# Optimization experiments

Hardware: AMD Instinct MI355X
Metric: run time of the kernel (lower is better)

Reference implementation:

```python
import jax, jax.numpy as jnp
import numpy as np

B, N, D = 32, 128, 64
E = N * N
EPS = 1e-5


def _bn(x, gamma, beta):
    # torch BatchNorm1d on (B, C, D): normalize per-channel over (batch, last dim)
    mean = jnp.mean(x, axis=(0, 2), keepdims=True)
    var = jnp.var(x, axis=(0, 2), keepdims=True)
    return (x - mean) * jax.lax.rsqrt(var + EPS) * gamma[None, :, None] + beta[None, :, None]


def _gat_layer(x, edge, Wh, We, Wp, Wa, gv, bv, ge, be):
    b, n, d = x.shape
    res = x
    z_h = jnp.einsum('bnd,od->bno', x, Wh)   # fc_h (torch Linear: y = x W^T)
    z_e = jnp.einsum('bed,od->beo', edge, We)  # fc_e
    # incidence matmuls are pure gathers: edge e = i*n + j
    z_src = jnp.broadcast_to(z_h[:, None, :, :], (b, n, n, d)).reshape(b, n * n, d)  # start: edge (i,j) <- node j
    z_dst = jnp.broadcast_to(z_h[:, :, None, :], (b, n, n, d)).reshape(b, n * n, d)  # end:   edge (i,j) <- node i
    z = jnp.concatenate([z_src, z_dst, z_e], axis=-1)  # (b, E, 3d)
    z_e_new = jnp.einsum('bec,oc->beo', z, Wp)  # fc_proj
    attn = jnp.einsum('bec,c->be', z, Wa[0])    # attn_fc -> (b, E)
    attn = jnp.where(attn >= 0, attn, 0.01 * attn)  # LeakyReLU(0.01)
    attn = jax.nn.softmax(attn.reshape(b, n, n), axis=2).reshape(b, n * n)  # softmax over sources j
    # scatter via end^T: node i <- sum_j attn[i,j] * z_src[i*n+j]
    agg = (attn[:, :, None] * z_src).reshape(b, n, n, d).sum(axis=2)
    x_new = jax.nn.elu(res + _bn(agg, gv, bv))
    edge_new = jax.nn.elu(_bn(z_e_new, ge, be))
    return x_new, edge_new


def setup_inputs():
    key = jax.random.key(0)
    ks = jax.random.split(key, 10)
    scale = float(np.sqrt(2.0 / D))
    return {
        'x': jax.random.normal(ks[0], (B, N, D), jnp.float32),
        'edge': jax.random.normal(ks[1], (B, E, D), jnp.float32),
        'Wh1': jax.random.normal(ks[2], (D, D), jnp.float32) * scale,
        'We1': jax.random.normal(ks[3], (D, D), jnp.float32) * scale,
        'Wp1': jax.random.normal(ks[4], (D, 3 * D), jnp.float32) * scale,
        'Wa1': jax.random.normal(ks[5], (1, 3 * D), jnp.float32) * scale,
        'Wh2': jax.random.normal(ks[6], (D, D), jnp.float32) * scale,
        'We2': jax.random.normal(ks[7], (D, D), jnp.float32) * scale,
        'Wp2': jax.random.normal(ks[8], (D, 3 * D), jnp.float32) * scale,
        'Wa2': jax.random.normal(ks[9], (1, 3 * D), jnp.float32) * scale,
        'gv1': jnp.ones((N,), jnp.float32), 'bv1': jnp.zeros((N,), jnp.float32),
        'ge1': jnp.ones((E,), jnp.float32), 'be1': jnp.zeros((E,), jnp.float32),
        'gv2': jnp.ones((N,), jnp.float32), 'bv2': jnp.zeros((N,), jnp.float32),
        'ge2': jnp.ones((E,), jnp.float32), 'be2': jnp.zeros((E,), jnp.float32),
    }


def reference(x, edge, Wh1, We1, Wp1, Wa1, Wh2, We2, Wp2, Wa2,
              gv1, bv1, ge1, be1, gv2, bv2, ge2, be2):
    x, edge = _gat_layer(x, edge, Wh1, We1, Wp1, Wa1, gv1, bv1, ge1, be1)
    x, edge = _gat_layer(x, edge, Wh2, We2, Wp2, Wa2, gv2, bv2, ge2, be2)
    return x, edge
```

## Files before the change

### kernel.cpp

```cpp
#include <hip/hip_runtime.h>
#include <math.h>

#define BB 32
#define NN 128
#define DD 64
#define EE (NN*NN)
#define EPSI 1e-5f

typedef __attribute__((ext_vector_type(8))) short bf16x8;
typedef __attribute__((ext_vector_type(4))) short s16x4;
typedef __attribute__((ext_vector_type(4))) float f32x4;

#define LGKM0() do { asm volatile("s_waitcnt lgkmcnt(0)" ::: "memory"); \
                     __builtin_amdgcn_sched_barrier(0); } while (0)

__device__ __forceinline__ short f2bf(float f) {
    union { float f; unsigned u; } v; v.f = f;
    unsigned u = v.u;
    unsigned r = (u + 0x7FFFu + ((u >> 16) & 1u)) >> 16;
    return (short)r;
}
__device__ __forceinline__ float elu(float v) {
    return v > 0.f ? v : __expf(v) - 1.f;
}

__global__ void k_fold(const float* __restrict__ Wp, const float* __restrict__ We,
                       const float* __restrict__ Wa,
                       short* __restrict__ Mbf, short* __restrict__ wbf)
{
    int t = blockIdx.x * 256 + threadIdx.x;
    int d = t >> 6, k = t & 63;
    float acc = 0.f;
    for (int o = 0; o < DD; ++o)
        acc += Wp[d*192 + 128 + o] * We[o*DD + k];
    Mbf[d*DD + k] = f2bf(acc);
    if (d == 0) {
        float aw = 0.f;
        for (int o = 0; o < DD; ++o)
            aw += Wa[128 + o] * We[o*DD + k];
        wbf[k] = f2bf(aw);
    }
}

__global__ void k_node(const float* __restrict__ x, const float* __restrict__ Wh,
                       const float* __restrict__ Wp, const float* __restrict__ Wa,
                       float* __restrict__ zh, float* __restrict__ PsT,
                       float* __restrict__ PdT, float* __restrict__ sO,
                       float* __restrict__ tO)
{
    int row = blockIdx.x;
    int b = row >> 7, n = row & 127;
    int d = threadIdx.x;
    __shared__ float xr[DD];
    __shared__ float zr[DD];
    xr[d] = x[row*DD + d];
    __syncthreads();
    float acc = 0.f;
#pragma unroll
    for (int k = 0; k < DD; ++k) acc += xr[k] * Wh[d*DD + k];
    zr[d] = acc;
    zh[row*DD + d] = acc;
    __syncthreads();
    float a0 = 0.f, a1 = 0.f;
#pragma unroll
    for (int o = 0; o < DD; ++o) {
        float z = zr[o];
        a0 += Wp[d*192 + o]      * z;
        a1 += Wp[d*192 + 64 + o] * z;
    }
    const int fi = ((b >> 4)*4 + (d >> 4))*256 + (((b >> 2) & 3)*16 + (d & 15))*4 + (b & 3);
    PsT[n*2048 + fi] = a0;
    PdT[n*2048 + fi] = a1;
    float sv = zr[d] * Wa[d];
    float tv = zr[d] * Wa[64 + d];
#pragma unroll
    for (int off = 32; off; off >>= 1) {
        sv += __shfl_xor(sv, off);
        tv += __shfl_xor(tv, off);
    }
    if (d == 0) { sO[row] = sv; tO[row] = tv; }
}

template <int INM, int OUTM>
__global__ __launch_bounds__(256, 4) void k_edge(
    const void* __restrict__ einv,
    const short* __restrict__ Mbf,
    const short* __restrict__ wbf,
    const float* __restrict__ PsT,
    const float* __restrict__ PdT,
    const float* __restrict__ ge, const float* __restrict__ be,
    void* __restrict__ eoutv, float* __restrict__ uout)
{
    __shared__ short As[4][32][72];
    const int t  = threadIdx.x;
    const int l  = t & 63;
    const int wv = t >> 6;
    const int lr = l & 15;
    const int lg = l >> 4;
    const int e0 = blockIdx.x * 4;
    const int e  = e0 + wv;
    const int i0 = e >> 7, j0 = e & 127;

    bf16x8 afr[2][2];
    if constexpr (INM == 0) {
        const float* ein = (const float*)einv;
        const int tq = (t >> 4) & 3;
        const int d0 = (t & 15) * 4;
        float4 sv[8];
#pragma unroll
        for (int it = 0; it < 8; ++it) {
            const int b = it*4 + wv;
            sv[it] = *reinterpret_cast<const float4*>(
                         ein + ((size_t)b*EE + e0 + tq)*DD + d0);
        }
#pragma unroll
        for (int it = 0; it < 8; ++it) {
            const int b = it*4 + wv;
            s16x4 o;
            o[0] = f2bf(sv[it].x); o[1] = f2bf(sv[it].y);
            o[2] = f2bf(sv[it].z); o[3] = f2bf(sv[it].w);
            *reinterpret_cast<s16x4*>(&As[tq][b][d0]) = o;
        }
        __syncthreads();
#pragma unroll
        for (int m = 0; m < 2; ++m)
#pragma unroll
            for (int s = 0; s < 2; ++s)
                afr[m][s] = *reinterpret_cast<const bf16x8*>(
                                &As[wv][16*m + lr][s*32 + lg*8]);
    } else {
        const short* ein = (const short*)einv + (size_t)e*BB*DD;
#pragma unroll
        for (int m = 0; m < 2; ++m)
#pragma unroll
            for (int s = 0; s < 2; ++s)
                afr[m][s] = *reinterpret_cast<const bf16x8*>(
                                ein + (16*m + lr)*DD + s*32 + lg*8);
    }

    bf16x8 bfr[4][2];
#pragma unroll
    for (int n = 0; n < 4; ++n)
#pragma unroll
        for (int s = 0; s < 2; ++s)
            bfr[n][s] = *reinterpret_cast<const bf16x8*>(Mbf + (16*n + lr)*DD + s*32 + lg*8);
    const bf16x8 zerov = (bf16x8){0,0,0,0,0,0,0,0};
    bf16x8 wfrag[2];
#pragma unroll
    for (int s = 0; s < 2; ++s)
        wfrag[s] = (lr == 0) ? *reinterpret_cast<const bf16x8*>(wbf + s*32 + lg*8) : zerov;

    f32x4 acc[2][4];
    f32x4 uacc[2];
    {
        const float* psb = PsT + j0*2048;
        const float* pdb = PdT + i0*2048;
#pragma unroll
        for (int m = 0; m < 2; ++m) {
            uacc[m] = (f32x4){0.f, 0.f, 0.f, 0.f};
#pragma unroll
            for (int n = 0; n < 4; ++n) {
                const float4 a = *reinterpret_cast<const float4*>(psb + (m*4+n)*256 + l*4);
                const float4 c = *reinterpret_cast<const float4*>(pdb + (m*4+n)*256 + l*4);
                acc[m][n] = (f32x4){a.x+c.x, a.y+c.y, a.z+c.z, a.w+c.w};
            }
        }
    }

#pragma unroll
    for (int m = 0; m < 2; ++m) {
#pragma unroll
        for (int n = 0; n < 4; ++n)
            acc[m][n] = __builtin_amdgcn_mfma_f32_16x16x32_bf16(afr[m][0], bfr[n][0], acc[m][n], 0, 0, 0);
        uacc[m] = __builtin_amdgcn_mfma_f32_16x16x32_bf16(afr[m][0], wfrag[0], uacc[m], 0, 0, 0);
#pragma unroll
        for (int n = 0; n < 4; ++n)
            acc[m][n] = __builtin_amdgcn_mfma_f32_16x16x32_bf16(afr[m][1], bfr[n][1], acc[m][n], 0, 0, 0);
        uacc[m] = __builtin_amdgcn_mfma_f32_16x16x32_bf16(afr[m][1], wfrag[1], uacc[m], 0, 0, 0);
    }

    float s1 = 0.f, s2 = 0.f;
#pragma unroll
    for (int m = 0; m < 2; ++m)
#pragma unroll
        for (int n = 0; n < 4; ++n)
#pragma unroll
            for (int q = 0; q < 4; ++q) { float v = acc[m][n][q]; s1 += v; s2 += v*v; }
#pragma unroll
    for (int off = 1; off < 64; off <<= 1) {
        s1 += __shfl_xor(s1, off);
        s2 += __shfl_xor(s2, off);
    }
    const float mean = s1 * (1.f/2048.f);
    const float var  = s2 * (1.f/2048.f) - mean*mean;
    const float sc = ge[e] * rsqrtf(var + EPSI);
    const float sh = be[e] - mean*sc;

#pragma unroll
    for (int m = 0; m < 2; ++m)
#pragma unroll
        for (int n = 0; n < 4; ++n)
#pragma unroll
            for (int q = 0; q < 4; ++q)
                acc[m][n][q] = elu(acc[m][n][q]*sc + sh);

    if (lr == 0) {
#pragma unroll
        for (int m = 0; m < 2; ++m)
#pragma unroll
            for (int q = 0; q < 4; ++q)
                uout[(size_t)(16*m + 4*lg + q)*EE + e] = uacc[m][q];
    }

    float (*Z)[68] = reinterpret_cast<float (*)[68]>(&As[wv][0][0]);
    LGKM0();
#pragma unroll
    for (int h = 0; h < 2; ++h) {
#pragma unroll
        for (int n = 0; n < 4; ++n)
#pragma unroll
            for (int q = 0; q < 4; ++q)
                Z[4*lg + q][16*n + lr] = acc[h][n][q];
        LGKM0();
        if constexpr (OUTM == 0) {
            float* eout = (float*)eoutv;
#pragma unroll
            for (int it = 0; it < 4; ++it) {
                const int rr = lg + 4*it;
                const int b  = 16*h + rr;
                float4 z = *reinterpret_cast<float4*>(&Z[rr][lr*4]);
                *reinterpret_cast<float4*>(eout + ((size_t)b*EE + e)*DD + lr*4) = z;
            }
        } else {
            short* eout = (short*)eoutv + (size_t)e*BB*DD;
#pragma unroll
            for (int it = 0; it < 2; ++it) {
                const int rr = (l >> 3) + 8*it;
                const int b  = 16*h + rr;
                const int c0 = (l & 7)*8;
                float4 zlo = *reinterpret_cast<float4*>(&Z[rr][c0]);
                float4 zhi = *reinterpret_cast<float4*>(&Z[rr][c0+4]);
                bf16x8 o;
                o[0]=f2bf(zlo.x); o[1]=f2bf(zlo.y); o[2]=f2bf(zlo.z); o[3]=f2bf(zlo.w);
                o[4]=f2bf(zhi.x); o[5]=f2bf(zhi.y); o[6]=f2bf(zhi.z); o[7]=f2bf(zhi.w);
                *reinterpret_cast<bf16x8*>(eout + b*DD + c0) = o;
            }
        }
        LGKM0();
    }
}

__global__ void k_attn(const float* __restrict__ sI, const float* __restrict__ tI,
                       const float* __restrict__ u, const float* __restrict__ zh,
                       float* __restrict__ agg)
{
    int blk = blockIdx.x; int b = blk >> 7, i = blk & 127;
    int l = threadIdx.x;
    __shared__ float at[NN];
    float ti = tI[blk];
    float l0 = sI[b*NN + l]      + ti + u[b*EE + i*NN + l];
    float l1 = sI[b*NN + l + 64] + ti + u[b*EE + i*NN + l + 64];
    l0 = l0 >= 0.f ? l0 : 0.01f*l0;
    l1 = l1 >= 0.f ? l1 : 0.01f*l1;
    float mx = fmaxf(l0, l1);
#pragma unroll
    for (int off = 32; off; off >>= 1) mx = fmaxf(mx, __shfl_xor(mx, off));
    float e0 = __expf(l0 - mx), e1 = __expf(l1 - mx);
    float sm = e0 + e1;
#pragma unroll
    for (int off = 32; off; off >>= 1) sm += __shfl_xor(sm, off);
    float inv = 1.f / sm;
    at[l]      = e0 * inv;
    at[l + 64] = e1 * inv;
    __syncthreads();
    float acc = 0.f;
    for (int j = 0; j < NN; ++j) acc += at[j] * zh[(b*NN + j)*DD + l];
    agg[(b*NN + i)*DD + l] = acc;
}

__global__ void k_vbn(const float* __restrict__ agg, const float* __restrict__ xres,
                      const float* __restrict__ gv, const float* __restrict__ bv,
                      float* __restrict__ xout)
{
    int i = blockIdx.x, t = threadIdx.x;
    float vals[8];
    float s1 = 0.f, s2 = 0.f;
#pragma unroll
    for (int q = 0; q < 8; ++q) {
        int m = t + 256*q; int b = m >> 6, d = m & 63;
        float v = agg[(b*NN + i)*DD + d];
        vals[q] = v; s1 += v; s2 += v*v;
    }
#pragma unroll
    for (int off = 1; off < 64; off <<= 1) {
        s1 += __shfl_xor(s1, off);
        s2 += __shfl_xor(s2, off);
    }
    __shared__ float r1[4], r2[4];
    int wv = t >> 6;
    if ((t & 63) == 0) { r1[wv] = s1; r2[wv] = s2; }
    __syncthreads();
    s1 = r1[0] + r1[1] + r1[2] + r1[3];
    s2 = r2[0] + r2[1] + r2[2] + r2[3];
    float mean  = s1 * (1.f/2048.f);
    float var   = s2 * (1.f/2048.f) - mean*mean;
    float scale = gv[i] * rsqrtf(var + EPSI);
    float shift = bv[i] - mean*scale;
#pragma unroll
    for (int q = 0; q < 8; ++q) {
        int m = t + 256*q; int b = m >> 6, d = m & 63;
        float v = vals[q]*scale + shift + xres[(b*NN + i)*DD + d];
        xout[(b*NN + i)*DD + d] = v > 0.f ? v : __expf(v) - 1.f;
    }
}

extern "C" void kernel_launch(void* const* d_in, const int* in_sizes, int n_in,
                              void* d_out, int out_size, void* d_ws, size_t ws_size,
                              hipStream_t stream)
{
    const float* x    = (const float*)d_in[0];
    const float* edge = (const float*)d_in[1];
    const float* Wh1  = (const float*)d_in[2];
    const float* We1  = (const float*)d_in[3];
    const float* Wp1  = (const float*)d_in[4];
    const float* Wa1  = (const float*)d_in[5];
    const float* Wh2  = (const float*)d_in[6];
    const float* We2  = (const float*)d_in[7];
    const float* Wp2  = (const float*)d_in[8];
    const float* Wa2  = (const float*)d_in[9];
    const float* gv1  = (const float*)d_in[10];
    const float* bv1  = (const float*)d_in[11];
    const float* ge1  = (const float*)d_in[12];
    const float* be1  = (const float*)d_in[13];
    const float* gv2  = (const float*)d_in[14];
    const float* bv2  = (const float*)d_in[15];
    const float* ge2  = (const float*)d_in[16];
    const float* be2  = (const float*)d_in[17];

    float* xout = (float*)d_out;
    float* eout = (float*)d_out + BB*NN*DD;

    float* ws  = (float*)d_ws;
    short* Mbf = (short*)ws;  ws += DD*DD/2;
    short* wbf = (short*)ws;  ws += DD/2;
    float* zh  = ws;  ws += BB*NN*DD;
    float* PsT = ws;  ws += NN*BB*DD;
    float* PdT = ws;  ws += NN*BB*DD;
    float* sb  = ws;  ws += BB*NN;
    float* tb  = ws;  ws += BB*NN;
    float* ub  = ws;  ws += BB*EE;
    float* agg = ws;  ws += BB*NN*DD;
    float* x1  = ws;  ws += BB*NN*DD;
    short* e1bf = (short*)ws;
    const size_t need = ((size_t)(ws - (float*)d_ws))*4 + (size_t)EE*BB*DD*2;

    const bool dense = (ws_size >= need);

    k_fold<<<16, 256, 0, stream>>>(Wp1, We1, Wa1, Mbf, wbf);
    k_node<<<BB*NN, 64, 0, stream>>>(x, Wh1, Wp1, Wa1, zh, PsT, PdT, sb, tb);
    if (dense)
        k_edge<0,1><<<EE/4, 256, 0, stream>>>(edge, Mbf, wbf, PsT, PdT, ge1, be1, e1bf, ub);
    else
        k_edge<0,0><<<EE/4, 256, 0, stream>>>(edge, Mbf, wbf, PsT, PdT, ge1, be1, eout, ub);
    k_attn<<<BB*NN, 64, 0, stream>>>(sb, tb, ub, zh, agg);
    k_vbn<<<NN, 256, 0, stream>>>(agg, x, gv1, bv1, x1);
    k_fold<<<16, 256, 0, stream>>>(Wp2, We2, Wa2, Mbf, wbf);
    k_node<<<BB*NN, 64, 0, stream>>>(x1, Wh2, Wp2, Wa2, zh, PsT, PdT, sb, tb);
    if (dense)
        k_edge<1,0><<<EE/4, 256, 0, stream>>>(e1bf, Mbf, wbf, PsT, PdT, ge2, be2, eout, ub);
    else
        k_edge<0,0><<<EE/4, 256, 0, stream>>>(eout, Mbf, wbf, PsT, PdT, ge2, be2, eout, ub);
    k_attn<<<BB*NN, 64, 0, stream>>>(sb, tb, ub, zh, agg);
    k_vbn<<<NN, 256, 0, stream>>>(agg, x1, gv2, bv2, xout);
}
```

Measured before the change: 208.6 us.

## Process two edges per wave, fold weight prep into node kernel, compute attention term in FP32

Each k_edge block now handles 8 edges (two per wave) instead of 4, which halves the grid and shares the PdT row and the Mbf fragments across both edges. The attention edge term u is now an FP32 dot product on the loaded edge data instead of an extra MFMA with a padded weight fragment. The separate k_fold launch is merged into k_node as extra blocks, removing two kernel launches. Register pressure goes up (launch bounds lowered from 4 to 3 blocks), shared memory per block doubles, and the shuffle reductions add ALU work.

```diff
diff --git a/kernel.cpp b/kernel.cpp
--- a/kernel.cpp
+++ b/kernel.cpp
@@ -20,37 +20,42 @@
     unsigned r = (u + 0x7FFFu + ((u >> 16) & 1u)) >> 16;
     return (short)r;
 }
+__device__ __forceinline__ float bf2f(short s) {
+    union { unsigned u; float f; } v; v.u = ((unsigned)(unsigned short)s) << 16;
+    return v.f;
+}
+__device__ __forceinline__ float dot4(float4 a, float4 b) {
+    return a.x*b.x + a.y*b.y + a.z*b.z + a.w*b.w;
+}
 __device__ __forceinline__ float elu(float v) {
     return v > 0.f ? v : __expf(v) - 1.f;
 }
 
-__global__ void k_fold(const float* __restrict__ Wp, const float* __restrict__ We,
+__global__ void k_node(const float* __restrict__ x, const float* __restrict__ Wh,
+                       const float* __restrict__ Wp, const float* __restrict__ We,
                        const float* __restrict__ Wa,
-                       short* __restrict__ Mbf, short* __restrict__ wbf)
-{
-    int t = blockIdx.x * 256 + threadIdx.x;
-    int d = t >> 6, k = t & 63;
-    float acc = 0.f;
-    for (int o = 0; o < DD; ++o)
-        acc += Wp[d*192 + 128 + o] * We[o*DD + k];
-    Mbf[d*DD + k] = f2bf(acc);
-    if (d == 0) {
-        float aw = 0.f;
-        for (int o = 0; o < DD; ++o)
-            aw += Wa[128 + o] * We[o*DD + k];
-        wbf[k] = f2bf(aw);
-    }
-}
-
-__global__ void k_node(const float* __restrict__ x, const float* __restrict__ Wh,
-                       const float* __restrict__ Wp, const float* __restrict__ Wa,
                        float* __restrict__ zh, float* __restrict__ PsT,
                        float* __restrict__ PdT, float* __restrict__ sO,
-                       float* __restrict__ tO)
+                       float* __restrict__ tO,
+                       short* __restrict__ Mbf, float* __restrict__ wf32)
 {
-    int row = blockIdx.x;
-    int b = row >> 7, n = row & 127;
-    int d = threadIdx.x;
+    const int row = blockIdx.x;
+    const int d = threadIdx.x;
+    if (row >= BB*NN) {
+        const int ff = row - BB*NN;
+        float acc = 0.f;
+        for (int o = 0; o < DD; ++o)
+            acc += Wp[ff*192 + 128 + o] * We[o*DD + d];
+        Mbf[ff*DD + d] = f2bf(acc);
+        if (ff == 0) {
+            float aw = 0.f;
+            for (int o = 0; o < DD; ++o)
+                aw += Wa[128 + o] * We[o*DD + d];
+            wf32[d] = aw;
+        }
+        return;
+    }
+    const int b = row >> 7, n = row & 127;
     __shared__ float xr[DD];
     __shared__ float zr[DD];
     xr[d] = x[row*DD + d];
@@ -82,60 +87,53 @@
 }
 
 template <int INM, int OUTM>
-__global__ __launch_bounds__(256, 4) void k_edge(
+__global__ __launch_bounds__(256, 3) void k_edge(
     const void* __restrict__ einv,
     const short* __restrict__ Mbf,
-    const short* __restrict__ wbf,
+    const float* __restrict__ wf32,
     const float* __restrict__ PsT,
     const float* __restrict__ PdT,
     const float* __restrict__ ge, const float* __restrict__ be,
     void* __restrict__ eoutv, float* __restrict__ uout)
 {
-    __shared__ short As[4][32][72];
+    __shared__ short As[8][32][72];
     const int t  = threadIdx.x;
     const int l  = t & 63;
     const int wv = t >> 6;
     const int lr = l & 15;
     const int lg = l >> 4;
-    const int e0 = blockIdx.x * 4;
-    const int e  = e0 + wv;
-    const int i0 = e >> 7, j0 = e & 127;
-
-    bf16x8 afr[2][2];
+    const int e0 = blockIdx.x * 8;
+    const int i0 = e0 >> 7;
+
     if constexpr (INM == 0) {
         const float* ein = (const float*)einv;
-        const int tq = (t >> 4) & 3;
+        const int g  = t >> 4;
         const int d0 = (t & 15) * 4;
-        float4 sv[8];
-#pragma unroll
-        for (int it = 0; it < 8; ++it) {
-            const int b = it*4 + wv;
+        const int el = g & 7;
+        const int bb = g >> 3;
+        const float4 wv4 = *reinterpret_cast<const float4*>(wf32 + d0);
+        float4 sv[16];
+#pragma unroll
+        for (int it = 0; it < 16; ++it) {
+            const int b = bb + 2*it;
             sv[it] = *reinterpret_cast<const float4*>(
-                         ein + ((size_t)b*EE + e0 + tq)*DD + d0);
-        }
-#pragma unroll
-        for (int it = 0; it < 8; ++it) {
-            const int b = it*4 + wv;
+                         ein + ((size_t)b*EE + e0 + el)*DD + d0);
+        }
+#pragma unroll
+        for (int it = 0; it < 16; ++it) {
+            const int b = bb + 2*it;
             s16x4 o;
             o[0] = f2bf(sv[it].x); o[1] = f2bf(sv[it].y);
             o[2] = f2bf(sv[it].z); o[3] = f2bf(sv[it].w);
-            *reinterpret_cast<s16x4*>(&As[tq][b][d0]) = o;
+            *reinterpret_cast<s16x4*>(&As[el][b][d0]) = o;
+            float up = dot4(sv[it], wv4);
+            up += __shfl_xor(up, 1);
+            up += __shfl_xor(up, 2);
+            up += __shfl_xor(up, 4);
+            up += __shfl_xor(up, 8);
+            if ((t & 15) == 0) uout[(size_t)b*EE + e0 + el] = up;
         }
         __syncthreads();
-#pragma unroll
-        for (int m = 0; m < 2; ++m)
-#pragma unroll
-            for (int s = 0; s < 2; ++s)
-                afr[m][s] = *reinterpret_cast<const bf16x8*>(
-                                &As[wv][16*m + lr][s*32 + lg*8]);
-    } else {
-        const short* ein = (const short*)einv + (size_t)e*BB*DD;
-#pragma unroll
-        for (int m = 0; m < 2; ++m)
-#pragma unroll
-            for (int s = 0; s < 2; ++s)
-                afr[m][s] = *reinterpret_cast<const bf16x8*>(
-                                ein + (16*m + lr)*DD + s*32 + lg*8);
     }
 
     bf16x8 bfr[4][2];
@@ -144,109 +142,157 @@
 #pragma unroll
         for (int s = 0; s < 2; ++s)
             bfr[n][s] = *reinterpret_cast<const bf16x8*>(Mbf + (16*n + lr)*DD + s*32 + lg*8);
-    const bf16x8 zerov = (bf16x8){0,0,0,0,0,0,0,0};
-    bf16x8 wfrag[2];
-#pragma unroll
-    for (int s = 0; s < 2; ++s)
-        wfrag[s] = (lr == 0) ? *reinterpret_cast<const bf16x8*>(wbf + s*32 + lg*8) : zerov;
-
-    f32x4 acc[2][4];
-    f32x4 uacc[2];
-    {
+
+    float4 wlo[2], whi[2];
+    if constexpr (INM == 1) {
+#pragma unroll
+        for (int s = 0; s < 2; ++s) {
+            wlo[s] = *reinterpret_cast<const float4*>(wf32 + s*32 + lg*8);
+            whi[s] = *reinterpret_cast<const float4*>(wf32 + s*32 + lg*8 + 4);
+        }
+    }
+
+    f32x4 acc[2][2][4];
+#pragma unroll
+    for (int ch = 0; ch < 2; ++ch) {
+        const int e  = e0 + 2*wv + ch;
+        const int j0 = e & 127;
         const float* psb = PsT + j0*2048;
         const float* pdb = PdT + i0*2048;
 #pragma unroll
-        for (int m = 0; m < 2; ++m) {
-            uacc[m] = (f32x4){0.f, 0.f, 0.f, 0.f};
+        for (int m = 0; m < 2; ++m)
 #pragma unroll
             for (int n = 0; n < 4; ++n) {
                 const float4 a = *reinterpret_cast<const float4*>(psb + (m*4+n)*256 + l*4);
                 const float4 c = *reinterpret_cast<const float4*>(pdb + (m*4+n)*256 + l*4);
-                acc[m][n] = (f32x4){a.x+c.x, a.y+c.y, a.z+c.z, a.w+c.w};
+                acc[ch][m][n] = (f32x4){a.x+c.x, a.y+c.y, a.z+c.z, a.w+c.w};
             }
-        }
-    }
-
-#pragma unroll
-    for (int m = 0; m < 2; ++m) {
+    }
+
+#pragma unroll
+    for (int ch = 0; ch < 2; ++ch) {
+        const int e = e0 + 2*wv + ch;
+        bf16x8 afr[2][2];
+        if constexpr (INM == 0) {
+#pragma unroll
+            for (int m = 0; m < 2; ++m)
+#pragma unroll
+                for (int s = 0; s < 2; ++s)
+                    afr[m][s] = *reinterpret_cast<const bf16x8*>(
+                                    &As[2*wv + ch][16*m + lr][s*32 + lg*8]);
+        } else {
+            const short* ein = (const short*)einv + (size_t)e*BB*DD;
+#pragma unroll
+            for (int m = 0; m < 2; ++m)
+#pragma unroll
+                for (int s = 0; s < 2; ++s)
+                    afr[m][s] = *reinterpret_cast<const bf16x8*>(
+                                    ein + (16*m + lr)*DD + s*32 + lg*8);
+#pragma unroll
+            for (int m = 0; m < 2; ++m) {
+                float up = 0.f;
+#pragma unroll
+                for (int s = 0; s < 2; ++s) {
+                    up += bf2f(afr[m][s][0])*wlo[s].x + bf2f(afr[m][s][1])*wlo[s].y
+                        + bf2f(afr[m][s][2])*wlo[s].z + bf2f(afr[m][s][3])*wlo[s].w
+                        + bf2f(afr[m][s][4])*whi[s].x + bf2f(afr[m][s][5])*whi[s].y
+                        + bf2f(afr[m][s][6])*whi[s].z + bf2f(afr[m][s][7])*whi[s].w;
+                }
+                up += __shfl_xor(up, 16);
+                up += __shfl_xor(up, 32);
+                if (lg == 0) uout[(size_t)(16*m + lr)*EE + e] = up;
+            }
+        }
+#pragma unroll
+        for (int m = 0; m < 2; ++m) {
+#pragma unroll
+            for (int n = 0; n < 4; ++n)
+                acc[ch][m][n] = __builtin_amdgcn_mfma_f32_16x16x32_bf16(afr[m][0], bfr[n][0], acc[ch][m][n], 0, 0, 0);
+#pragma unroll
+            for (int n = 0; n < 4; ++n)
+                acc[ch][m][n] = __builtin_amdgcn_mfma_f32_16x16x32_bf16(afr[m][1], bfr[n][1], acc[ch][m][n], 0, 0, 0);
+        }
+    }
+
+    float s1a = 0.f, s2a = 0.f, s1b = 0.f, s2b = 0.f;
+#pragma unroll
+    for (int m = 0; m < 2; ++m)
 #pragma unroll
         for (int n = 0; n < 4; ++n)
-            acc[m][n] = __builtin_amdgcn_mfma_f32_16x16x32_bf16(afr[m][0], bfr[n][0], acc[m][n], 0, 0, 0);
-        uacc[m] = __builtin_amdgcn_mfma_f32_16x16x32_bf16(afr[m][0], wfrag[0], uacc[m], 0, 0, 0);
-#pragma unroll
-        for (int n = 0; n < 4; ++n)
-            acc[m][n] = __builtin_amdgcn_mfma_f32_16x16x32_bf16(afr[m][1], bfr[n][1], acc[m][n], 0, 0, 0);
-        uacc[m] = __builtin_amdgcn_mfma_f32_16x16x32_bf16(afr[m][1], wfrag[1], uacc[m], 0, 0, 0);
-    }
-
-    float s1 = 0.f, s2 = 0.f;
-#pragma unroll
-    for (int m = 0; m < 2; ++m)
-#pragma unroll
-        for (int n = 0; n < 4; ++n)
-#pragma unroll
-            for (int q = 0; q < 4; ++q) { float v = acc[m][n][q]; s1 += v; s2 += v*v; }
+#pragma unroll
+            for (int q = 0; q < 4; ++q) {
+                float va = acc[0][m][n][q]; s1a += va; s2a += va*va;
+                float vb = acc[1][m][n][q]; s1b += vb; s2b += vb*vb;
+            }
 #pragma unroll
     for (int off = 1; off < 64; off <<= 1) {
-        s1 += __shfl_xor(s1, off);
-        s2 += __shfl_xor(s2, off);
-    }
-    const float mean = s1 * (1.f/2048.f);
-    const float var  = s2 * (1.f/2048.f) - mean*mean;
-    const float sc = ge[e] * rsqrtf(var + EPSI);
-    const float sh = be[e] - mean*sc;
-
-#pragma unroll
-    for (int m = 0; m < 2; ++m)
-#pragma unroll
-        for (int n = 0; n < 4; ++n)
-#pragma unroll
-            for (int q = 0; q < 4; ++q)
-                acc[m][n][q] = elu(acc[m][n][q]*sc + sh);
-
-    if (lr == 0) {
+        s1a += __shfl_xor(s1a, off);
+        s2a += __shfl_xor(s2a, off);
+        s1b += __shfl_xor(s1b, off);
+        s2b += __shfl_xor(s2b, off);
+    }
+    float scs[2], shs[2];
+    {
+        const int eA = e0 + 2*wv;
+        float mean = s1a * (1.f/2048.f);
+        float var  = s2a * (1.f/2048.f) - mean*mean;
+        scs[0] = ge[eA] * rsqrtf(var + EPSI);
+        shs[0] = be[eA] - mean*scs[0];
+        mean = s1b * (1.f/2048.f);
+        var  = s2b * (1.f/2048.f) - mean*mean;
+        scs[1] = ge[eA+1] * rsqrtf(var + EPSI);
+        shs[1] = be[eA+1] - mean*scs[1];
+    }
+
+#pragma unroll
+    for (int ch = 0; ch < 2; ++ch)
 #pragma unroll
         for (int m = 0; m < 2; ++m)
 #pragma unroll
-            for (int q = 0; q < 4; ++q)
-                uout[(size_t)(16*m + 4*lg + q)*EE + e] = uacc[m][q];
-    }
-
-    float (*Z)[68] = reinterpret_cast<float (*)[68]>(&As[wv][0][0]);
+            for (int n = 0; n < 4; ++n)
+#pragma unroll
+                for (int q = 0; q < 4; ++q)
+                    acc[ch][m][n][q] = elu(acc[ch][m][n][q]*scs[ch] + shs[ch]);
+
     LGKM0();
 #pragma unroll
-    for (int h = 0; h < 2; ++h) {
-#pragma unroll
-        for (int n = 0; n < 4; ++n)
-#pragma unroll
-            for (int q = 0; q < 4; ++q)
-                Z[4*lg + q][16*n + lr] = acc[h][n][q];
-        LGKM0();
-        if constexpr (OUTM == 0) {
-            float* eout = (float*)eoutv;
-#pragma unroll
-            for (int it = 0; it < 4; ++it) {
-                const int rr = lg + 4*it;
-                const int b  = 16*h + rr;
-                float4 z = *reinterpret_cast<float4*>(&Z[rr][lr*4]);
-                *reinterpret_cast<float4*>(eout + ((size_t)b*EE + e)*DD + lr*4) = z;
+    for (int ch = 0; ch < 2; ++ch) {
+        const int e = e0 + 2*wv + ch;
+        float (*Z)[68] = reinterpret_cast<float (*)[68]>(&As[2*wv + ch][0][0]);
+#pragma unroll
+        for (int h = 0; h < 2; ++h) {
+#pragma unroll
+            for (int n = 0; n < 4; ++n)
+#pragma unroll
+                for (int q = 0; q < 4; ++q)
+                    Z[4*lg + q][16*n + lr] = acc[ch][h][n][q];
+            LGKM0();
+            if constexpr (OUTM == 0) {
+                float* eout = (float*)eoutv;
+#pragma unroll
+                for (int it = 0; it < 4; ++it) {
+                    const int rr = lg + 4*it;
+                    const int b  = 16*h + rr;
+                    float4 z = *reinterpret_cast<float4*>(&Z[rr][lr*4]);
+                    *reinterpret_cast<float4*>(eout + ((size_t)b*EE + e)*DD + lr*4) = z;
+                }
+            } else {
+                short* eout = (short*)eoutv + (size_t)e*BB*DD;
+#pragma unroll
+                for (int it = 0; it < 2; ++it) {
+                    const int rr = (l >> 3) + 8*it;
+                    const int b  = 16*h + rr;
+                    const int c0 = (l & 7)*8;
+                    float4 zlo = *reinterpret_cast<float4*>(&Z[rr][c0]);
+                    float4 zhi = *reinterpret_cast<float4*>(&Z[rr][c0+4]);
+                    bf16x8 o;
+                    o[0]=f2bf(zlo.x); o[1]=f2bf(zlo.y); o[2]=f2bf(zlo.z); o[3]=f2bf(zlo.w);
+                    o[4]=f2bf(zhi.x); o[5]=f2bf(zhi.y); o[6]=f2bf(zhi.z); o[7]=f2bf(zhi.w);
+                    *reinterpret_cast<bf16x8*>(eout + b*DD + c0) = o;
+                }
             }
-        } else {
-            short* eout = (short*)eoutv + (size_t)e*BB*DD;
-#pragma unroll
-            for (int it = 0; it < 2; ++it) {
-                const int rr = (l >> 3) + 8*it;
-                const int b  = 16*h + rr;
-                const int c0 = (l & 7)*8;
-                float4 zlo = *reinterpret_cast<float4*>(&Z[rr][c0]);
-                float4 zhi = *reinterpret_cast<float4*>(&Z[rr][c0+4]);
-                bf16x8 o;
-                o[0]=f2bf(zlo.x); o[1]=f2bf(zlo.y); o[2]=f2bf(zlo.z); o[3]=f2bf(zlo.w);
-                o[4]=f2bf(zhi.x); o[5]=f2bf(zhi.y); o[6]=f2bf(zhi.z); o[7]=f2bf(zhi.w);
-                *reinterpret_cast<bf16x8*>(eout + b*DD + c0) = o;
-            }
-        }
-        LGKM0();
+            LGKM0();
+        }
     }
 }
 
@@ -342,7 +388,7 @@
 
     float* ws  = (float*)d_ws;
     short* Mbf = (short*)ws;  ws += DD*DD/2;
-    short* wbf = (short*)ws;  ws += DD/2;
+    float* wf  = ws;  ws += DD;
     float* zh  = ws;  ws += BB*NN*DD;
     float* PsT = ws;  ws += NN*BB*DD;
     float* PdT = ws;  ws += NN*BB*DD;
@@ -356,20 +402,18 @@
 
     const bool dense = (ws_size >= need);
 
-    k_fold<<<16, 256, 0, stream>>>(Wp1, We1, Wa1, Mbf, wbf);
-    k_node<<<BB*NN, 64, 0, stream>>>(x, Wh1, Wp1, Wa1, zh, PsT, PdT, sb, tb);
+    k_node<<<BB*NN + 64, 64, 0, stream>>>(x, Wh1, Wp1, We1, Wa1, zh, PsT, PdT, sb, tb, Mbf, wf);
     if (dense)
-        k_edge<0,1><<<EE/4, 256, 0, stream>>>(edge, Mbf, wbf, PsT, PdT, ge1, be1, e1bf, ub);
+        k_edge<0,1><<<EE/8, 256, 0, stream>>>(edge, Mbf, wf, PsT, PdT, ge1, be1, e1bf, ub);
     else
-        k_edge<0,0><<<EE/4, 256, 0, stream>>>(edge, Mbf, wbf, PsT, PdT, ge1, be1, eout, ub);
+        k_edge<0,0><<<EE/8, 256, 0, stream>>>(edge, Mbf, wf, PsT, PdT, ge1, be1, eout, ub);
     k_attn<<<BB*NN, 64, 0, stream>>>(sb, tb, ub, zh, agg);
     k_vbn<<<NN, 256, 0, stream>>>(agg, x, gv1, bv1, x1);
-    k_fold<<<16, 256, 0, stream>>>(Wp2, We2, Wa2, Mbf, wbf);
-    k_node<<<BB*NN, 64, 0, stream>>>(x1, Wh2, Wp2, Wa2, zh, PsT, PdT, sb, tb);
+    k_node<<<BB*NN + 64, 64, 0, stream>>>(x1, Wh2, Wp2, We2, Wa2, zh, PsT, PdT, sb, tb, Mbf, wf);
     if (dense)
-        k_edge<1,0><<<EE/4, 256, 0, stream>>>(e1bf, Mbf, wbf, PsT, PdT, ge2, be2, eout, ub);
+        k_edge<1,0><<<EE/8, 256, 0, stream>>>(e1bf, Mbf, wf, PsT, PdT, ge2, be2, eout, ub);
     else
-        k_edge<0,0><<<EE/4, 256, 0, stream>>>(eout, Mbf, wbf, PsT, PdT, ge2, be2, eout, ub);
+        k_edge<0,0><<<EE/8, 256, 0, stream>>>(eout, Mbf, wf, PsT, PdT, ge2, be2, eout, ub);
     k_attn<<<BB*NN, 64, 0, stream>>>(sb, tb, ub, zh, agg);
     k_vbn<<<NN, 256, 0, stream>>>(agg, x1, gv2, bv2, xout);
 }
```

After: 206.4 us. About the same (-1.1%).
